# Optimization experiments

Hardware: AMD Instinct MI355X
Metric: run time of the kernel (lower is better)

The kernel has to match this reference:

```python
import jax, jax.numpy as jnp
import numpy as np

B, N, FIN, FOUT = 8, 2048, 128, 128


def setup_inputs() -> dict:
    key = jax.random.key(0)
    k1, k2, k3, k4, k5 = jax.random.split(key, 5)
    x = jax.random.normal(k1, (B, N, FIN), dtype=jnp.float32)
    adj = jax.random.randint(k2, (N, N), 0, 2, dtype=jnp.int32)
    # W stored [in, out] (transpose of torch Linear weight; same math via x @ W)
    W = jax.random.normal(k3, (FIN, FOUT), dtype=jnp.float32) * (1.0 / np.sqrt(FIN))
    # a: Linear(2*out, 1) split into src/dst halves: a([h_i,h_j]) = h_i@a_src + h_j@a_dst
    a_src = jax.random.normal(k4, (FOUT,), dtype=jnp.float32) * 0.1
    a_dst = jax.random.normal(k5, (FOUT,), dtype=jnp.float32) * 0.1
    return {"x": x, "adj": adj, "W": W, "a_src": a_src, "a_dst": a_dst}


def reference(x, adj, W, a_src, a_dst):
    # h: [B, N, FOUT]
    h = jnp.einsum('bnf,fo->bno', x, W)
    # attention logits e_ij = LeakyReLU(a_src.h_i + a_dst.h_j), built by broadcast
    s_i = jnp.einsum('bno,o->bn', h, a_src)  # [B, N]
    s_j = jnp.einsum('bno,o->bn', h, a_dst)  # [B, N]
    e = jax.nn.leaky_relu(s_i[:, :, None] + s_j[:, None, :], negative_slope=0.2)  # [B,N,N]
    scores = jnp.where(adj[None, :, :] == 0, -jnp.inf, e)
    attn = jax.nn.softmax(scores, axis=-1)
    attn = jnp.nan_to_num(attn, nan=0.0)  # rows with no neighbors -> all zeros
    # dropout is identity in eval mode
    out = jnp.einsum('bij,bjo->bio', attn, h)  # [B, N, FOUT]
    return out
```

## Files before the change

### kernel.cpp

```cpp
#include <hip/hip_runtime.h>
#include <math.h>

#define BATCH 8
#define NN 2048
#define FF 128

typedef __attribute__((ext_vector_type(4))) float f32x4;
typedef _Float16 half8 __attribute__((ext_vector_type(8)));

__device__ __forceinline__ unsigned short h2u(_Float16 h) {
    return __builtin_bit_cast(unsigned short, h);
}

__device__ __forceinline__ void h_split(float f, unsigned short& hi, unsigned short& lo) {
    const _Float16 hh = (_Float16)f;
    hi = h2u(hh);
    lo = h2u((_Float16)(f - (float)hh));
}

__global__ __launch_bounds__(512) void k_prep(const int* __restrict__ adj,
                                              const float* __restrict__ W,
                                              unsigned short* __restrict__ Wf_hi,
                                              unsigned short* __restrict__ Wf_lo,
                                              unsigned* __restrict__ amT) {
    const int t = threadIdx.x;
    if (blockIdx.x == 128) {
        #pragma unroll 4
        for (int e = 0; e < 32; ++e) {
            const int fi = e * 512 + t;
            const int j = fi & 7, lane = (fi >> 3) & 63, nt = (fi >> 9) & 7, ks = fi >> 12;
            const int k = ks * 32 + (lane >> 4) * 8 + j;
            const int col = nt * 16 + (lane & 15);
            unsigned short hh, hl;
            h_split(W[k * FF + col], hh, hl);
            Wf_hi[fi] = hh;
            Wf_lo[fi] = hl;
        }
    } else {
        const int w = t >> 6, lane = t & 63;
        const int row = blockIdx.x * 16 + w * 2;
        #pragma unroll
        for (int rr = 0; rr < 2; ++rr) {
            const int* __restrict__ ar = adj + (size_t)(row + rr) * NN;
            #pragma unroll 16
            for (int seg = 0; seg < 32; ++seg) {
                const unsigned long long m = __ballot(ar[seg * 64 + lane] != 0);
                if (lane == 0)  amT[(size_t)(seg * 2) * NN + row + rr] = (unsigned)m;
                if (lane == 32) amT[(size_t)(seg * 2 + 1) * NN + row + rr] = (unsigned)(m >> 32);
            }
        }
    }
}

__global__ __launch_bounds__(512) void k_h(const float* __restrict__ x,
                                           const unsigned short* __restrict__ Wf_hi,
                                           const unsigned short* __restrict__ Wf_lo,
                                           const float* __restrict__ a_src,
                                           const float* __restrict__ a_dst,
                                           unsigned short* __restrict__ hF,
                                           float* __restrict__ Eg,  float* __restrict__ E2g,
                                           float* __restrict__ Sg,  float* __restrict__ S2g) {
    __shared__ float sred[2][64];
    __shared__ float dred[2][64];

    const int t = threadIdx.x;
    const int w = t >> 6, lane = t & 63;
    const int mt = w >> 1, ch = w & 1;
    const int nl = lane & 15, quad = lane >> 4;
    const int row0 = blockIdx.x * 64;
    const int b = row0 >> 11, jloc0 = row0 & 2047;
    const int gr = row0 + mt * 16 + nl;

    f32x4 acc[4] = {{0.f,0.f,0.f,0.f},{0.f,0.f,0.f,0.f},{0.f,0.f,0.f,0.f},{0.f,0.f,0.f,0.f}};

    #pragma unroll
    for (int ks = 0; ks < 4; ++ks) {
        const float4 xa = *reinterpret_cast<const float4*>(&x[(size_t)gr * FF + ks * 32 + quad * 8]);
        const float4 xb = *reinterpret_cast<const float4*>(&x[(size_t)gr * FF + ks * 32 + quad * 8 + 4]);
        const float xv[8] = {xa.x, xa.y, xa.z, xa.w, xb.x, xb.y, xb.z, xb.w};
        half8 ah, al;
        #pragma unroll
        for (int i = 0; i < 8; ++i) {
            const _Float16 hh = (_Float16)xv[i];
            ah[i] = hh;
            al[i] = (_Float16)(xv[i] - (float)hh);
        }
        #pragma unroll
        for (int nt = 0; nt < 4; ++nt) {
            const int gnt = ch * 4 + nt;
            const int bo = ((ks * 8 + gnt) * 64 + lane) * 8;
            const half8 bh = *reinterpret_cast<const half8*>(&Wf_hi[bo]);
            const half8 bl = *reinterpret_cast<const half8*>(&Wf_lo[bo]);
            acc[nt] = __builtin_amdgcn_mfma_f32_16x16x32_f16(ah, bh, acc[nt], 0, 0, 0);
            acc[nt] = __builtin_amdgcn_mfma_f32_16x16x32_f16(al, bh, acc[nt], 0, 0, 0);
            acc[nt] = __builtin_amdgcn_mfma_f32_16x16x32_f16(ah, bl, acc[nt], 0, 0, 0);
        }
    }

    const int jloc = jloc0 + mt * 16 + quad * 4;
    const int jg = jloc >> 3, u0 = jloc & 7;
    #pragma unroll
    for (int nt = 0; nt < 4; ++nt) {
        const int gnt = ch * 4 + nt;
        ushort4 hv;
        hv.x = h2u((_Float16)acc[nt][0]);
        hv.y = h2u((_Float16)acc[nt][1]);
        hv.z = h2u((_Float16)acc[nt][2]);
        hv.w = h2u((_Float16)acc[nt][3]);
        *reinterpret_cast<ushort4*>(&hF[(size_t)b * 262144 + gnt * 32768 + jg * 128 + nl * 8 + u0]) = hv;
    }

    float as[4], ad[4];
    #pragma unroll
    for (int nt = 0; nt < 4; ++nt) {
        const int col = ch * 64 + nt * 16 + nl;
        as[nt] = a_src[col];
        ad[nt] = a_dst[col];
    }
    #pragma unroll
    for (int r = 0; r < 4; ++r) {
        float sp = acc[0][r] * as[0] + acc[1][r] * as[1] + acc[2][r] * as[2] + acc[3][r] * as[3];
        float dp = acc[0][r] * ad[0] + acc[1][r] * ad[1] + acc[2][r] * ad[2] + acc[3][r] * ad[3];
        #pragma unroll
        for (int off = 8; off >= 1; off >>= 1) {
            sp += __shfl_xor(sp, off, 16);
            dp += __shfl_xor(dp, off, 16);
        }
        if (nl == 0) {
            sred[ch][mt * 16 + quad * 4 + r] = sp;
            dred[ch][mt * 16 + quad * 4 + r] = dp;
        }
    }
    __syncthreads();
    if (t < 64) {
        const float sp = sred[0][t] + sred[1][t];
        const float dp = dred[0][t] + dred[1][t];
        const int row = row0 + t;
        Sg[row]  = __expf(sp - 2.f);
        S2g[row] = __expf(0.2f * sp - 2.f);
        Eg[row]  = __expf(dp - 2.f);
        E2g[row] = __expf(0.2f * dp - 2.f);
    }
}

__global__ __launch_bounds__(512, 2) void k_attn(const unsigned short* __restrict__ hF,
                                                 const unsigned* __restrict__ amT,
                                                 const float* __restrict__ Eg,
                                                 const float* __restrict__ E2g,
                                                 const float* __restrict__ Sg,
                                                 const float* __restrict__ S2g,
                                                 float* __restrict__ out) {
    __shared__ float E_l[NN];
    __shared__ float E2_l[NN];
    __shared__ unsigned am_l[64 * 64];
    __shared__ unsigned short pA[2][64 * 72];

    const int t = threadIdx.x;
    const int b = blockIdx.y;
    const int i0 = blockIdx.x * 64;

    *reinterpret_cast<float4*>(&E_l[t * 4])  = *reinterpret_cast<const float4*>(&Eg[(size_t)b * NN + t * 4]);
    *reinterpret_cast<float4*>(&E2_l[t * 4]) = *reinterpret_cast<const float4*>(&E2g[(size_t)b * NN + t * 4]);
    #pragma unroll
    for (int k = 0; k < 8; ++k) {
        const int idx = k * 512 + t;
        am_l[idx] = amT[(size_t)(idx >> 6) * NN + i0 + (idx & 63)];
    }
    __syncthreads();

    const int rp = t >> 4, jw4 = t & 15;
    const int ra = rp * 2, rb = ra + 1;
    const float Sa  = Sg[(size_t)b * NN + i0 + ra];
    const float S2a = S2g[(size_t)b * NN + i0 + ra];
    const float Sb  = Sg[(size_t)b * NN + i0 + rb];
    const float S2b = S2g[(size_t)b * NN + i0 + rb];
    const int bitb = (jw4 & 7) * 4;
    const int pwo = ra * 72 + jw4 * 4;

    const int w = t >> 6, lane = t & 63;
    const int nl = lane & 15, quad = lane >> 4;
    const int mtp = w & 1, ntp = w >> 1;
    const unsigned short* __restrict__ hFb = hF + (size_t)b * 262144;
    int bofs[2], aofs[2];
    #pragma unroll
    for (int nn = 0; nn < 2; ++nn) bofs[nn] = (ntp + nn * 4) * 32768 + quad * 128 + nl * 8;
    #pragma unroll
    for (int mm = 0; mm < 2; ++mm) aofs[mm] = ((mtp + mm * 2) * 16 + nl) * 72 + quad * 8;

    f32x4 acc[2][2] = {{{0.f,0.f,0.f,0.f},{0.f,0.f,0.f,0.f}},{{0.f,0.f,0.f,0.f},{0.f,0.f,0.f,0.f}}};
    f32x4 lac[2] = {{0.f,0.f,0.f,0.f},{0.f,0.f,0.f,0.f}};
    half8 ones;
    #pragma unroll
    for (int i = 0; i < 8; ++i) ones[i] = (_Float16)1.f;

    for (int tt = 0; tt < 32; ++tt) {
        const int jt = tt * 64;
        const int buf = tt & 1;
        const int jofs = jt * 16;

        half8 bfr[2][2];
        #pragma unroll
        for (int nn = 0; nn < 2; ++nn) {
            bfr[nn][0] = *reinterpret_cast<const half8*>(hFb + bofs[nn] + jofs);
            bfr[nn][1] = *reinterpret_cast<const half8*>(hFb + bofs[nn] + jofs + 512);
        }

        {
            const int jb = jt + jw4 * 4;
            const float4 ej4  = *reinterpret_cast<const float4*>(&E_l[jb]);
            const float4 e2j4 = *reinterpret_cast<const float4*>(&E2_l[jb]);
            const uint2 mw = *reinterpret_cast<const uint2*>(&am_l[(tt * 2 + (jw4 >> 3)) * 64 + ra]);
            const float ejA[4]  = {ej4.x, ej4.y, ej4.z, ej4.w};
            const float e2jA[4] = {e2j4.x, e2j4.y, e2j4.z, e2j4.w};
            ushort4 ha, hb;
            #pragma unroll
            for (int jj = 0; jj < 4; ++jj) {
                const float ua = fmaxf(Sa * ejA[jj], S2a * e2jA[jj]);
                const float ub = fmaxf(Sb * ejA[jj], S2b * e2jA[jj]);
                const float pa = ((mw.x >> (bitb + jj)) & 1u) ? ua : 0.f;
                const float pb = ((mw.y >> (bitb + jj)) & 1u) ? ub : 0.f;
                ((unsigned short*)&ha)[jj] = h2u((_Float16)pa);
                ((unsigned short*)&hb)[jj] = h2u((_Float16)pb);
            }
            *reinterpret_cast<ushort4*>(&pA[buf][pwo]) = ha;
            *reinterpret_cast<ushort4*>(&pA[buf][pwo + 72]) = hb;
        }

        __syncthreads();

        half8 afr[2][2];
        #pragma unroll
        for (int mm = 0; mm < 2; ++mm) {
            afr[mm][0] = *reinterpret_cast<const half8*>(&pA[buf][aofs[mm]]);
            afr[mm][1] = *reinterpret_cast<const half8*>(&pA[buf][aofs[mm] + 32]);
        }
        #pragma unroll
        for (int mm = 0; mm < 2; ++mm) {
            #pragma unroll
            for (int kh = 0; kh < 2; ++kh) {
                lac[mm] = __builtin_amdgcn_mfma_f32_16x16x32_f16(afr[mm][kh], ones, lac[mm], 0, 0, 0);
                acc[mm][0] = __builtin_amdgcn_mfma_f32_16x16x32_f16(afr[mm][kh], bfr[0][kh], acc[mm][0], 0, 0, 0);
                acc[mm][1] = __builtin_amdgcn_mfma_f32_16x16x32_f16(afr[mm][kh], bfr[1][kh], acc[mm][1], 0, 0, 0);
            }
        }
    }

    #pragma unroll
    for (int mm = 0; mm < 2; ++mm) {
        const int row = i0 + (mtp + mm * 2) * 16 + quad * 4;
        #pragma unroll
        for (int r = 0; r < 4; ++r) {
            const float l = lac[mm][r];
            const float inv = (l > 0.f) ? 1.f / l : 0.f;
            #pragma unroll
            for (int nn = 0; nn < 2; ++nn) {
                const int col = (ntp + nn * 4) * 16 + nl;
                out[((size_t)b * NN + row + r) * FF + col] = acc[mm][nn][r] * inv;
            }
        }
    }
}

extern "C" void kernel_launch(void* const* d_in, const int* in_sizes, int n_in,
                              void* d_out, int out_size, void* d_ws, size_t ws_size,
                              hipStream_t stream) {
    const float* x     = (const float*)d_in[0];
    const int*   adj   = (const int*)d_in[1];
    const float* W     = (const float*)d_in[2];
    const float* a_src = (const float*)d_in[3];
    const float* a_dst = (const float*)d_in[4];
    float* out = (float*)d_out;

    unsigned short* hF    = (unsigned short*)d_ws;
    unsigned short* Wf_hi = hF + 2097152;
    unsigned short* Wf_lo = Wf_hi + 16384;
    float* Eg  = (float*)(Wf_lo + 16384);
    float* E2g = Eg + 16384;
    float* Sg  = E2g + 16384;
    float* S2g = Sg + 16384;
    unsigned* amT = (unsigned*)(S2g + 16384);

    k_prep<<<129, 512, 0, stream>>>(adj, W, Wf_hi, Wf_lo, amT);
    k_h<<<256, 512, 0, stream>>>(x, Wf_hi, Wf_lo, a_src, a_dst, hF, Eg, E2g, Sg, S2g);
    k_attn<<<dim3(NN / 64, BATCH), 512, 0, stream>>>(hF, amT, Eg, E2g, Sg, S2g, out);
}
```

Before: 124.2 us.

## Fuse three kernels into one cooperative persistent kernel with grid syncs

Merges the prep, projection, and attention kernels into a single cooperative launch of 256 blocks that separates the phases with grid-wide syncs. The three-kernel path is kept as a fallback if the cooperative launch fails. The adjacency bit-packing and W split work are also redistributed evenly over all 256 blocks. The aim is to remove inter-kernel launch gaps and tail effects, at the cost of grid-sync overhead and a larger shared-memory footprint during the early phases, which could limit occupancy.

```diff
diff --git a/kernel.cpp b/kernel.cpp
--- a/kernel.cpp
+++ b/kernel.cpp
@@ -1,9 +1,12 @@
 #include <hip/hip_runtime.h>
+#include <hip/hip_cooperative_groups.h>
 #include <math.h>
 
 #define BATCH 8
 #define NN 2048
 #define FF 128
+
+namespace cg = cooperative_groups;
 
 typedef __attribute__((ext_vector_type(4))) float f32x4;
 typedef _Float16 half8 __attribute__((ext_vector_type(8)));
@@ -18,56 +21,50 @@
     lo = h2u((_Float16)(f - (float)hh));
 }
 
-__global__ __launch_bounds__(512) void k_prep(const int* __restrict__ adj,
-                                              const float* __restrict__ W,
-                                              unsigned short* __restrict__ Wf_hi,
-                                              unsigned short* __restrict__ Wf_lo,
-                                              unsigned* __restrict__ amT) {
-    const int t = threadIdx.x;
-    if (blockIdx.x == 128) {
-        #pragma unroll 4
-        for (int e = 0; e < 32; ++e) {
-            const int fi = e * 512 + t;
-            const int j = fi & 7, lane = (fi >> 3) & 63, nt = (fi >> 9) & 7, ks = fi >> 12;
-            const int k = ks * 32 + (lane >> 4) * 8 + j;
-            const int col = nt * 16 + (lane & 15);
+__device__ __forceinline__ void phaseA(int bx, int t,
+                                       const int* __restrict__ adj,
+                                       const float* __restrict__ W,
+                                       unsigned short* __restrict__ Wf_hi,
+                                       unsigned short* __restrict__ Wf_lo,
+                                       unsigned* __restrict__ amT) {
+    const int w = t >> 6, lane = t & 63;
+    const int row = bx * 8 + w;
+    const int* __restrict__ ar = adj + (size_t)row * NN;
+    #pragma unroll 8
+    for (int seg = 0; seg < 32; ++seg) {
+        const unsigned long long m = __ballot(ar[seg * 64 + lane] != 0);
+        if (lane == 0)  amT[(size_t)(seg * 2) * NN + row] = (unsigned)m;
+        if (lane == 32) amT[(size_t)(seg * 2 + 1) * NN + row] = (unsigned)(m >> 32);
+    }
+    if (bx < 8) {
+        #pragma unroll
+        for (int e = 0; e < 4; ++e) {
+            const int fi = bx * 2048 + e * 512 + t;
+            const int j = fi & 7, ln = (fi >> 3) & 63, nt = (fi >> 9) & 7, ks = fi >> 12;
+            const int k = ks * 32 + (ln >> 4) * 8 + j;
+            const int col = nt * 16 + (ln & 15);
             unsigned short hh, hl;
             h_split(W[k * FF + col], hh, hl);
             Wf_hi[fi] = hh;
             Wf_lo[fi] = hl;
         }
-    } else {
-        const int w = t >> 6, lane = t & 63;
-        const int row = blockIdx.x * 16 + w * 2;
-        #pragma unroll
-        for (int rr = 0; rr < 2; ++rr) {
-            const int* __restrict__ ar = adj + (size_t)(row + rr) * NN;
-            #pragma unroll 16
-            for (int seg = 0; seg < 32; ++seg) {
-                const unsigned long long m = __ballot(ar[seg * 64 + lane] != 0);
-                if (lane == 0)  amT[(size_t)(seg * 2) * NN + row + rr] = (unsigned)m;
-                if (lane == 32) amT[(size_t)(seg * 2 + 1) * NN + row + rr] = (unsigned)(m >> 32);
-            }
-        }
-    }
-}
-
-__global__ __launch_bounds__(512) void k_h(const float* __restrict__ x,
-                                           const unsigned short* __restrict__ Wf_hi,
-                                           const unsigned short* __restrict__ Wf_lo,
-                                           const float* __restrict__ a_src,
-                                           const float* __restrict__ a_dst,
-                                           unsigned short* __restrict__ hF,
-                                           float* __restrict__ Eg,  float* __restrict__ E2g,
-                                           float* __restrict__ Sg,  float* __restrict__ S2g) {
-    __shared__ float sred[2][64];
-    __shared__ float dred[2][64];
-
-    const int t = threadIdx.x;
+    }
+}
+
+__device__ __forceinline__ void phaseB(int bx, int t,
+                                       const float* __restrict__ x,
+                                       const unsigned short* __restrict__ Wf_hi,
+                                       const unsigned short* __restrict__ Wf_lo,
+                                       const float* __restrict__ a_src,
+                                       const float* __restrict__ a_dst,
+                                       unsigned short* __restrict__ hF,
+                                       float* __restrict__ Eg, float* __restrict__ E2g,
+                                       float* __restrict__ Sg, float* __restrict__ S2g,
+                                       float* __restrict__ sred, float* __restrict__ dred) {
     const int w = t >> 6, lane = t & 63;
+    const int nl = lane & 15, quad = lane >> 4;
     const int mt = w >> 1, ch = w & 1;
-    const int nl = lane & 15, quad = lane >> 4;
-    const int row0 = blockIdx.x * 64;
+    const int row0 = bx * 64;
     const int b = row0 >> 11, jloc0 = row0 & 2047;
     const int gr = row0 + mt * 16 + nl;
 
@@ -127,14 +124,14 @@
             dp += __shfl_xor(dp, off, 16);
         }
         if (nl == 0) {
-            sred[ch][mt * 16 + quad * 4 + r] = sp;
-            dred[ch][mt * 16 + quad * 4 + r] = dp;
+            sred[ch * 64 + mt * 16 + quad * 4 + r] = sp;
+            dred[ch * 64 + mt * 16 + quad * 4 + r] = dp;
         }
     }
     __syncthreads();
     if (t < 64) {
-        const float sp = sred[0][t] + sred[1][t];
-        const float dp = dred[0][t] + dred[1][t];
+        const float sp = sred[t] + sred[64 + t];
+        const float dp = dred[t] + dred[64 + t];
         const int row = row0 + t;
         Sg[row]  = __expf(sp - 2.f);
         S2g[row] = __expf(0.2f * sp - 2.f);
@@ -143,21 +140,18 @@
     }
 }
 
-__global__ __launch_bounds__(512, 2) void k_attn(const unsigned short* __restrict__ hF,
-                                                 const unsigned* __restrict__ amT,
-                                                 const float* __restrict__ Eg,
-                                                 const float* __restrict__ E2g,
-                                                 const float* __restrict__ Sg,
-                                                 const float* __restrict__ S2g,
-                                                 float* __restrict__ out) {
-    __shared__ float E_l[NN];
-    __shared__ float E2_l[NN];
-    __shared__ unsigned am_l[64 * 64];
-    __shared__ unsigned short pA[2][64 * 72];
-
-    const int t = threadIdx.x;
-    const int b = blockIdx.y;
-    const int i0 = blockIdx.x * 64;
+__device__ __forceinline__ void phaseC(int bx, int t,
+                                       const unsigned short* __restrict__ hF,
+                                       const unsigned* __restrict__ amT,
+                                       const float* __restrict__ Eg, const float* __restrict__ E2g,
+                                       const float* __restrict__ Sg, const float* __restrict__ S2g,
+                                       float* __restrict__ out,
+                                       float* __restrict__ E_l, float* __restrict__ E2_l,
+                                       unsigned* __restrict__ am_l, unsigned short* __restrict__ pA) {
+    const int b = bx >> 5;
+    const int i0 = (bx & 31) * 64;
+    const int w = t >> 6, lane = t & 63;
+    const int nl = lane & 15, quad = lane >> 4;
 
     *reinterpret_cast<float4*>(&E_l[t * 4])  = *reinterpret_cast<const float4*>(&Eg[(size_t)b * NN + t * 4]);
     *reinterpret_cast<float4*>(&E2_l[t * 4]) = *reinterpret_cast<const float4*>(&E2g[(size_t)b * NN + t * 4]);
@@ -177,8 +171,6 @@
     const int bitb = (jw4 & 7) * 4;
     const int pwo = ra * 72 + jw4 * 4;
 
-    const int w = t >> 6, lane = t & 63;
-    const int nl = lane & 15, quad = lane >> 4;
     const int mtp = w & 1, ntp = w >> 1;
     const unsigned short* __restrict__ hFb = hF + (size_t)b * 262144;
     int bofs[2], aofs[2];
@@ -222,8 +214,8 @@
                 ((unsigned short*)&ha)[jj] = h2u((_Float16)pa);
                 ((unsigned short*)&hb)[jj] = h2u((_Float16)pb);
             }
-            *reinterpret_cast<ushort4*>(&pA[buf][pwo]) = ha;
-            *reinterpret_cast<ushort4*>(&pA[buf][pwo + 72]) = hb;
+            *reinterpret_cast<ushort4*>(&pA[buf * 4608 + pwo]) = ha;
+            *reinterpret_cast<ushort4*>(&pA[buf * 4608 + pwo + 72]) = hb;
         }
 
         __syncthreads();
@@ -231,8 +223,8 @@
         half8 afr[2][2];
         #pragma unroll
         for (int mm = 0; mm < 2; ++mm) {
-            afr[mm][0] = *reinterpret_cast<const half8*>(&pA[buf][aofs[mm]]);
-            afr[mm][1] = *reinterpret_cast<const half8*>(&pA[buf][aofs[mm] + 32]);
+            afr[mm][0] = *reinterpret_cast<const half8*>(&pA[buf * 4608 + aofs[mm]]);
+            afr[mm][1] = *reinterpret_cast<const half8*>(&pA[buf * 4608 + aofs[mm] + 32]);
         }
         #pragma unroll
         for (int mm = 0; mm < 2; ++mm) {
@@ -259,6 +251,65 @@
             }
         }
     }
+}
+
+__global__ __launch_bounds__(512, 2) void k_fused(
+        const float* __restrict__ x, const int* __restrict__ adj,
+        const float* __restrict__ W, const float* __restrict__ a_src,
+        const float* __restrict__ a_dst,
+        unsigned short* __restrict__ Wf_hi, unsigned short* __restrict__ Wf_lo,
+        unsigned short* __restrict__ hF,
+        float* __restrict__ Eg, float* __restrict__ E2g,
+        float* __restrict__ Sg, float* __restrict__ S2g,
+        unsigned* __restrict__ amT, float* __restrict__ out) {
+    __shared__ float E_l[NN];
+    __shared__ float E2_l[NN];
+    __shared__ unsigned am_l[64 * 64];
+    __shared__ unsigned short pA[2 * 64 * 72];
+    __shared__ float sred[2 * 64];
+    __shared__ float dred[2 * 64];
+
+    cg::grid_group grid = cg::this_grid();
+    const int bx = blockIdx.x, t = threadIdx.x;
+
+    phaseA(bx, t, adj, W, Wf_hi, Wf_lo, amT);
+    grid.sync();
+    phaseB(bx, t, x, Wf_hi, Wf_lo, a_src, a_dst, hF, Eg, E2g, Sg, S2g, sred, dred);
+    grid.sync();
+    phaseC(bx, t, hF, amT, Eg, E2g, Sg, S2g, out, E_l, E2_l, am_l, pA);
+}
+
+__global__ __launch_bounds__(512) void k_pA(const int* __restrict__ adj,
+                                            const float* __restrict__ W,
+                                            unsigned short* __restrict__ Wf_hi,
+                                            unsigned short* __restrict__ Wf_lo,
+                                            unsigned* __restrict__ amT) {
+    phaseA(blockIdx.x, threadIdx.x, adj, W, Wf_hi, Wf_lo, amT);
+}
+
+__global__ __launch_bounds__(512, 2) void k_pB(const float* __restrict__ x,
+                                               const unsigned short* __restrict__ Wf_hi,
+                                               const unsigned short* __restrict__ Wf_lo,
+                                               const float* __restrict__ a_src,
+                                               const float* __restrict__ a_dst,
+                                               unsigned short* __restrict__ hF,
+                                               float* __restrict__ Eg, float* __restrict__ E2g,
+                                               float* __restrict__ Sg, float* __restrict__ S2g) {
+    __shared__ float sred[2 * 64];
+    __shared__ float dred[2 * 64];
+    phaseB(blockIdx.x, threadIdx.x, x, Wf_hi, Wf_lo, a_src, a_dst, hF, Eg, E2g, Sg, S2g, sred, dred);
+}
+
+__global__ __launch_bounds__(512, 2) void k_pC(const unsigned short* __restrict__ hF,
+                                               const unsigned* __restrict__ amT,
+                                               const float* __restrict__ Eg, const float* __restrict__ E2g,
+                                               const float* __restrict__ Sg, const float* __restrict__ S2g,
+                                               float* __restrict__ out) {
+    __shared__ float E_l[NN];
+    __shared__ float E2_l[NN];
+    __shared__ unsigned am_l[64 * 64];
+    __shared__ unsigned short pA[2 * 64 * 72];
+    phaseC(blockIdx.x, threadIdx.x, hF, amT, Eg, E2g, Sg, S2g, out, E_l, E2_l, am_l, pA);
 }
 
 extern "C" void kernel_launch(void* const* d_in, const int* in_sizes, int n_in,
@@ -280,7 +331,15 @@
     float* S2g = Sg + 16384;
     unsigned* amT = (unsigned*)(S2g + 16384);
 
-    k_prep<<<129, 512, 0, stream>>>(adj, W, Wf_hi, Wf_lo, amT);
-    k_h<<<256, 512, 0, stream>>>(x, Wf_hi, Wf_lo, a_src, a_dst, hF, Eg, E2g, Sg, S2g);
-    k_attn<<<dim3(NN / 64, BATCH), 512, 0, stream>>>(hF, amT, Eg, E2g, Sg, S2g, out);
-}
+    void* args[] = {(void*)&x, (void*)&adj, (void*)&W, (void*)&a_src, (void*)&a_dst,
+                    (void*)&Wf_hi, (void*)&Wf_lo, (void*)&hF,
+                    (void*)&Eg, (void*)&E2g, (void*)&Sg, (void*)&S2g,
+                    (void*)&amT, (void*)&out};
+    hipError_t err = hipLaunchCooperativeKernel((const void*)k_fused, dim3(256), dim3(512),
+                                                args, 0, stream);
+    if (err != hipSuccess) {
+        k_pA<<<256, 512, 0, stream>>>(adj, W, Wf_hi, Wf_lo, amT);
+        k_pB<<<256, 512, 0, stream>>>(x, Wf_hi, Wf_lo, a_src, a_dst, hF, Eg, E2g, Sg, S2g);
+        k_pC<<<256, 512, 0, stream>>>(hF, amT, Eg, E2g, Sg, S2g, out);
+    }
+}
```

New measurement: 173.1 us. 1.39x slower.

## Split attention over neighbor dimension into two halves and combine partials

Applied to the files above, without the earlier changes.

The attention kernel now splits the j (neighbor) range into two halves via a third grid dimension, writing unnormalized partial outputs and row sums to workspace. A new combine kernel adds the partials and normalizes. The prep and h kernels are re-gridded into smaller blocks for more parallelism. The aim is to double the attention block count and raise occupancy (launch bound 4) on a 256-CU device, at the cost of an extra kernel launch and extra global traffic for the partials.

```diff
diff --git a/kernel.cpp b/kernel.cpp
--- a/kernel.cpp
+++ b/kernel.cpp
@@ -18,41 +18,39 @@
     lo = h2u((_Float16)(f - (float)hh));
 }
 
-__global__ __launch_bounds__(512) void k_prep(const int* __restrict__ adj,
+__global__ __launch_bounds__(256) void k_prep(const int* __restrict__ adj,
                                               const float* __restrict__ W,
                                               unsigned short* __restrict__ Wf_hi,
                                               unsigned short* __restrict__ Wf_lo,
                                               unsigned* __restrict__ amT) {
     const int t = threadIdx.x;
-    if (blockIdx.x == 128) {
-        #pragma unroll 4
-        for (int e = 0; e < 32; ++e) {
-            const int fi = e * 512 + t;
-            const int j = fi & 7, lane = (fi >> 3) & 63, nt = (fi >> 9) & 7, ks = fi >> 12;
-            const int k = ks * 32 + (lane >> 4) * 8 + j;
-            const int col = nt * 16 + (lane & 15);
+    const int bx = blockIdx.x;
+    if (bx < 512) {
+        const int w = t >> 6, lane = t & 63;
+        const int row = bx * 4 + w;
+        const int* __restrict__ ar = adj + (size_t)row * NN;
+        #pragma unroll 8
+        for (int seg = 0; seg < 32; ++seg) {
+            const unsigned long long m = __ballot(ar[seg * 64 + lane] != 0);
+            if (lane == 0)  amT[(size_t)(seg * 2) * NN + row] = (unsigned)m;
+            if (lane == 32) amT[(size_t)(seg * 2 + 1) * NN + row] = (unsigned)(m >> 32);
+        }
+    } else {
+        #pragma unroll
+        for (int e = 0; e < 8; ++e) {
+            const int fi = (bx - 512) * 2048 + e * 256 + t;
+            const int j = fi & 7, ln = (fi >> 3) & 63, nt = (fi >> 9) & 7, ks = fi >> 12;
+            const int k = ks * 32 + (ln >> 4) * 8 + j;
+            const int col = nt * 16 + (ln & 15);
             unsigned short hh, hl;
             h_split(W[k * FF + col], hh, hl);
             Wf_hi[fi] = hh;
             Wf_lo[fi] = hl;
         }
-    } else {
-        const int w = t >> 6, lane = t & 63;
-        const int row = blockIdx.x * 16 + w * 2;
-        #pragma unroll
-        for (int rr = 0; rr < 2; ++rr) {
-            const int* __restrict__ ar = adj + (size_t)(row + rr) * NN;
-            #pragma unroll 16
-            for (int seg = 0; seg < 32; ++seg) {
-                const unsigned long long m = __ballot(ar[seg * 64 + lane] != 0);
-                if (lane == 0)  amT[(size_t)(seg * 2) * NN + row + rr] = (unsigned)m;
-                if (lane == 32) amT[(size_t)(seg * 2 + 1) * NN + row + rr] = (unsigned)(m >> 32);
-            }
-        }
-    }
-}
-
-__global__ __launch_bounds__(512) void k_h(const float* __restrict__ x,
+    }
+}
+
+__global__ __launch_bounds__(256) void k_h(const float* __restrict__ x,
                                            const unsigned short* __restrict__ Wf_hi,
                                            const unsigned short* __restrict__ Wf_lo,
                                            const float* __restrict__ a_src,
@@ -60,18 +58,18 @@
                                            unsigned short* __restrict__ hF,
                                            float* __restrict__ Eg,  float* __restrict__ E2g,
                                            float* __restrict__ Sg,  float* __restrict__ S2g) {
-    __shared__ float sred[2][64];
-    __shared__ float dred[2][64];
+    __shared__ float sred[4 * 16];
+    __shared__ float dred[4 * 16];
 
     const int t = threadIdx.x;
     const int w = t >> 6, lane = t & 63;
-    const int mt = w >> 1, ch = w & 1;
     const int nl = lane & 15, quad = lane >> 4;
-    const int row0 = blockIdx.x * 64;
+    const int row0 = blockIdx.x * 16;
     const int b = row0 >> 11, jloc0 = row0 & 2047;
-    const int gr = row0 + mt * 16 + nl;
-
-    f32x4 acc[4] = {{0.f,0.f,0.f,0.f},{0.f,0.f,0.f,0.f},{0.f,0.f,0.f,0.f},{0.f,0.f,0.f,0.f}};
+    const int gr = row0 + nl;
+    const int nt0 = w * 2;
+
+    f32x4 acc[2] = {{0.f,0.f,0.f,0.f},{0.f,0.f,0.f,0.f}};
 
     #pragma unroll
     for (int ks = 0; ks < 4; ++ks) {
@@ -86,55 +84,53 @@
             al[i] = (_Float16)(xv[i] - (float)hh);
         }
         #pragma unroll
-        for (int nt = 0; nt < 4; ++nt) {
-            const int gnt = ch * 4 + nt;
-            const int bo = ((ks * 8 + gnt) * 64 + lane) * 8;
+        for (int nn = 0; nn < 2; ++nn) {
+            const int bo = ((ks * 8 + nt0 + nn) * 64 + lane) * 8;
             const half8 bh = *reinterpret_cast<const half8*>(&Wf_hi[bo]);
             const half8 bl = *reinterpret_cast<const half8*>(&Wf_lo[bo]);
-            acc[nt] = __builtin_amdgcn_mfma_f32_16x16x32_f16(ah, bh, acc[nt], 0, 0, 0);
-            acc[nt] = __builtin_amdgcn_mfma_f32_16x16x32_f16(al, bh, acc[nt], 0, 0, 0);
-            acc[nt] = __builtin_amdgcn_mfma_f32_16x16x32_f16(ah, bl, acc[nt], 0, 0, 0);
-        }
-    }
-
-    const int jloc = jloc0 + mt * 16 + quad * 4;
+            acc[nn] = __builtin_amdgcn_mfma_f32_16x16x32_f16(ah, bh, acc[nn], 0, 0, 0);
+            acc[nn] = __builtin_amdgcn_mfma_f32_16x16x32_f16(al, bh, acc[nn], 0, 0, 0);
+            acc[nn] = __builtin_amdgcn_mfma_f32_16x16x32_f16(ah, bl, acc[nn], 0, 0, 0);
+        }
+    }
+
+    const int jloc = jloc0 + quad * 4;
     const int jg = jloc >> 3, u0 = jloc & 7;
     #pragma unroll
-    for (int nt = 0; nt < 4; ++nt) {
-        const int gnt = ch * 4 + nt;
+    for (int nn = 0; nn < 2; ++nn) {
         ushort4 hv;
-        hv.x = h2u((_Float16)acc[nt][0]);
-        hv.y = h2u((_Float16)acc[nt][1]);
-        hv.z = h2u((_Float16)acc[nt][2]);
-        hv.w = h2u((_Float16)acc[nt][3]);
-        *reinterpret_cast<ushort4*>(&hF[(size_t)b * 262144 + gnt * 32768 + jg * 128 + nl * 8 + u0]) = hv;
-    }
-
-    float as[4], ad[4];
-    #pragma unroll
-    for (int nt = 0; nt < 4; ++nt) {
-        const int col = ch * 64 + nt * 16 + nl;
-        as[nt] = a_src[col];
-        ad[nt] = a_dst[col];
+        hv.x = h2u((_Float16)acc[nn][0]);
+        hv.y = h2u((_Float16)acc[nn][1]);
+        hv.z = h2u((_Float16)acc[nn][2]);
+        hv.w = h2u((_Float16)acc[nn][3]);
+        *reinterpret_cast<ushort4*>(&hF[(size_t)b * 262144 + (nt0 + nn) * 32768 + jg * 128 + nl * 8 + u0]) = hv;
+    }
+
+    float as[2], ad[2];
+    #pragma unroll
+    for (int nn = 0; nn < 2; ++nn) {
+        const int col = (nt0 + nn) * 16 + nl;
+        as[nn] = a_src[col];
+        ad[nn] = a_dst[col];
     }
     #pragma unroll
     for (int r = 0; r < 4; ++r) {
-        float sp = acc[0][r] * as[0] + acc[1][r] * as[1] + acc[2][r] * as[2] + acc[3][r] * as[3];
-        float dp = acc[0][r] * ad[0] + acc[1][r] * ad[1] + acc[2][r] * ad[2] + acc[3][r] * ad[3];
+        float sp = acc[0][r] * as[0] + acc[1][r] * as[1];
+        float dp = acc[0][r] * ad[0] + acc[1][r] * ad[1];
         #pragma unroll
         for (int off = 8; off >= 1; off >>= 1) {
             sp += __shfl_xor(sp, off, 16);
             dp += __shfl_xor(dp, off, 16);
         }
         if (nl == 0) {
-            sred[ch][mt * 16 + quad * 4 + r] = sp;
-            dred[ch][mt * 16 + quad * 4 + r] = dp;
+            sred[w * 16 + quad * 4 + r] = sp;
+            dred[w * 16 + quad * 4 + r] = dp;
         }
     }
     __syncthreads();
-    if (t < 64) {
-        const float sp = sred[0][t] + sred[1][t];
-        const float dp = dred[0][t] + dred[1][t];
+    if (t < 16) {
+        const float sp = sred[t] + sred[16 + t] + sred[32 + t] + sred[48 + t];
+        const float dp = dred[t] + dred[16 + t] + dred[32 + t] + dred[48 + t];
         const int row = row0 + t;
         Sg[row]  = __expf(sp - 2.f);
         S2g[row] = __expf(0.2f * sp - 2.f);
@@ -143,28 +139,31 @@
     }
 }
 
-__global__ __launch_bounds__(512, 2) void k_attn(const unsigned short* __restrict__ hF,
+__global__ __launch_bounds__(512, 4) void k_attn(const unsigned short* __restrict__ hF,
                                                  const unsigned* __restrict__ amT,
                                                  const float* __restrict__ Eg,
                                                  const float* __restrict__ E2g,
                                                  const float* __restrict__ Sg,
                                                  const float* __restrict__ S2g,
-                                                 float* __restrict__ out) {
-    __shared__ float E_l[NN];
-    __shared__ float E2_l[NN];
-    __shared__ unsigned am_l[64 * 64];
-    __shared__ unsigned short pA[2][64 * 72];
+                                                 float* __restrict__ P,
+                                                 float* __restrict__ L) {
+    __shared__ float E_l[1024];
+    __shared__ float E2_l[1024];
+    __shared__ unsigned am_l[32 * 64];
+    __shared__ unsigned short pA[2 * 64 * 72];
 
     const int t = threadIdx.x;
     const int b = blockIdx.y;
     const int i0 = blockIdx.x * 64;
-
-    *reinterpret_cast<float4*>(&E_l[t * 4])  = *reinterpret_cast<const float4*>(&Eg[(size_t)b * NN + t * 4]);
-    *reinterpret_cast<float4*>(&E2_l[t * 4]) = *reinterpret_cast<const float4*>(&E2g[(size_t)b * NN + t * 4]);
-    #pragma unroll
-    for (int k = 0; k < 8; ++k) {
+    const int jh = blockIdx.z;
+    const int jbase = jh * 1024;
+
+    *reinterpret_cast<float2*>(&E_l[t * 2])  = *reinterpret_cast<const float2*>(&Eg[(size_t)b * NN + jbase + t * 2]);
+    *reinterpret_cast<float2*>(&E2_l[t * 2]) = *reinterpret_cast<const float2*>(&E2g[(size_t)b * NN + jbase + t * 2]);
+    #pragma unroll
+    for (int k = 0; k < 4; ++k) {
         const int idx = k * 512 + t;
-        am_l[idx] = amT[(size_t)(idx >> 6) * NN + i0 + (idx & 63)];
+        am_l[idx] = amT[(size_t)(jh * 32 + (idx >> 6)) * NN + i0 + (idx & 63)];
     }
     __syncthreads();
 
@@ -183,7 +182,7 @@
     const unsigned short* __restrict__ hFb = hF + (size_t)b * 262144;
     int bofs[2], aofs[2];
     #pragma unroll
-    for (int nn = 0; nn < 2; ++nn) bofs[nn] = (ntp + nn * 4) * 32768 + quad * 128 + nl * 8;
+    for (int nn = 0; nn < 2; ++nn) bofs[nn] = (ntp + nn * 4) * 32768 + (jbase + quad * 8) * 16 + nl * 8;
     #pragma unroll
     for (int mm = 0; mm < 2; ++mm) aofs[mm] = ((mtp + mm * 2) * 16 + nl) * 72 + quad * 8;
 
@@ -193,10 +192,9 @@
     #pragma unroll
     for (int i = 0; i < 8; ++i) ones[i] = (_Float16)1.f;
 
-    for (int tt = 0; tt < 32; ++tt) {
-        const int jt = tt * 64;
+    for (int tt = 0; tt < 16; ++tt) {
         const int buf = tt & 1;
-        const int jofs = jt * 16;
+        const int jofs = tt * 1024;
 
         half8 bfr[2][2];
         #pragma unroll
@@ -206,7 +204,7 @@
         }
 
         {
-            const int jb = jt + jw4 * 4;
+            const int jb = tt * 64 + jw4 * 4;
             const float4 ej4  = *reinterpret_cast<const float4*>(&E_l[jb]);
             const float4 e2j4 = *reinterpret_cast<const float4*>(&E2_l[jb]);
             const uint2 mw = *reinterpret_cast<const uint2*>(&am_l[(tt * 2 + (jw4 >> 3)) * 64 + ra]);
@@ -222,8 +220,8 @@
                 ((unsigned short*)&ha)[jj] = h2u((_Float16)pa);
                 ((unsigned short*)&hb)[jj] = h2u((_Float16)pb);
             }
-            *reinterpret_cast<ushort4*>(&pA[buf][pwo]) = ha;
-            *reinterpret_cast<ushort4*>(&pA[buf][pwo + 72]) = hb;
+            *reinterpret_cast<ushort4*>(&pA[buf * 4608 + pwo]) = ha;
+            *reinterpret_cast<ushort4*>(&pA[buf * 4608 + pwo + 72]) = hb;
         }
 
         __syncthreads();
@@ -231,8 +229,8 @@
         half8 afr[2][2];
         #pragma unroll
         for (int mm = 0; mm < 2; ++mm) {
-            afr[mm][0] = *reinterpret_cast<const half8*>(&pA[buf][aofs[mm]]);
-            afr[mm][1] = *reinterpret_cast<const half8*>(&pA[buf][aofs[mm] + 32]);
+            afr[mm][0] = *reinterpret_cast<const half8*>(&pA[buf * 4608 + aofs[mm]]);
+            afr[mm][1] = *reinterpret_cast<const half8*>(&pA[buf * 4608 + aofs[mm] + 32]);
         }
         #pragma unroll
         for (int mm = 0; mm < 2; ++mm) {
@@ -245,19 +243,39 @@
         }
     }
 
+    float* __restrict__ Pb = P + ((size_t)jh * BATCH + b) * 262144;
+    float* __restrict__ Lb = L + ((size_t)jh * BATCH + b) * 2048;
     #pragma unroll
     for (int mm = 0; mm < 2; ++mm) {
-        const int row = i0 + (mtp + mm * 2) * 16 + quad * 4;
+        const int lrow = (mtp + mm * 2) * 16 + quad * 4;
         #pragma unroll
         for (int r = 0; r < 4; ++r) {
-            const float l = lac[mm][r];
-            const float inv = (l > 0.f) ? 1.f / l : 0.f;
             #pragma unroll
             for (int nn = 0; nn < 2; ++nn) {
                 const int col = (ntp + nn * 4) * 16 + nl;
-                out[((size_t)b * NN + row + r) * FF + col] = acc[mm][nn][r] * inv;
+                Pb[(size_t)(i0 + lrow + r) * FF + col] = acc[mm][nn][r];
             }
-        }
+            if (nl == 0 && ntp == 0) Lb[i0 + lrow + r] = lac[mm][r];
+        }
+    }
+}
+
+__global__ __launch_bounds__(256) void k_comb(const float* __restrict__ P,
+                                              const float* __restrict__ L,
+                                              float* __restrict__ out) {
+    const int g0 = blockIdx.x * 512 + threadIdx.x;
+    #pragma unroll
+    for (int it = 0; it < 2; ++it) {
+        const int g = g0 + it * 256;
+        const size_t flat = (size_t)g * 4;
+        const int row = (int)(flat >> 7);
+        const float l = L[row] + L[16384 + row];
+        const float inv = (l > 0.f) ? 1.f / l : 0.f;
+        const float4 p0 = *reinterpret_cast<const float4*>(&P[flat]);
+        const float4 p1 = *reinterpret_cast<const float4*>(&P[2097152 + flat]);
+        *reinterpret_cast<float4*>(&out[flat]) =
+            make_float4((p0.x + p1.x) * inv, (p0.y + p1.y) * inv,
+                        (p0.z + p1.z) * inv, (p0.w + p1.w) * inv);
     }
 }
 
@@ -279,8 +297,11 @@
     float* Sg  = E2g + 16384;
     float* S2g = Sg + 16384;
     unsigned* amT = (unsigned*)(S2g + 16384);
-
-    k_prep<<<129, 512, 0, stream>>>(adj, W, Wf_hi, Wf_lo, amT);
-    k_h<<<256, 512, 0, stream>>>(x, Wf_hi, Wf_lo, a_src, a_dst, hF, Eg, E2g, Sg, S2g);
-    k_attn<<<dim3(NN / 64, BATCH), 512, 0, stream>>>(hF, amT, Eg, E2g, Sg, S2g, out);
-}
+    float* P = (float*)(amT + 131072);
+    float* L = P + 4194304;
+
+    k_prep<<<520, 256, 0, stream>>>(adj, W, Wf_hi, Wf_lo, amT);
+    k_h<<<1024, 256, 0, stream>>>(x, Wf_hi, Wf_lo, a_src, a_dst, hF, Eg, E2g, Sg, S2g);
+    k_attn<<<dim3(32, BATCH, 2), 512, 0, stream>>>(hF, amT, Eg, E2g, Sg, S2g, P, L);
+    k_comb<<<1024, 256, 0, stream>>>(P, L, out);
+}
```

Measured after the change: 117.6 us. -5.3%, faster.
